# Optimization experiments

Hardware: AMD Instinct MI355X
Metric: run time of the kernel (lower is better)

The kernel has to match this reference:

```python
import jax, jax.numpy as jnp
import numpy as np

BATCH = 4096
P = 64            # num_of_adc_p
L = 1024          # dense_sampling_L
LT = 256          # num_samples_L_tilde


def setup_inputs() -> dict:
    key = jax.random.key(0)
    kx, kw = jax.random.split(key)
    x = jax.random.normal(kx, (BATCH, P * L), dtype=jnp.float32)
    # weight emulates rounded/clamped learned sampling offsets in [1, L-1]
    weight = jax.random.randint(kw, (LT,), 1, L - 1, dtype=jnp.int64)
    return {
        "x": x,
        "weight": weight,
        "num_of_adc_p": P,
        "num_samples_L_tilde": LT,
        "dense_sampling_L": L,
    }


def reference(x, weight, num_of_adc_p, num_samples_L_tilde, dense_sampling_L):
    # out[:, i*LT + j] = x[:, i*L + weight[j]]  -> single fused gather
    # indices: [P, LT] -> flattened column gather
    cols = (jnp.arange(num_of_adc_p, dtype=weight.dtype)[:, None] * dense_sampling_L
            + weight[None, :]).reshape(-1)  # [P*LT]
    return jnp.take(x, cols, axis=1)  # [B, P*LT]
```

## Files before the change

kernel.cpp:

```cpp
#include <hip/hip_runtime.h>
#include <hip/hip_bf16.h>

#define BATCH 4096
#define P     64
#define L     1024
#define LT    256
#define NPAIRS (BATCH * P)

__global__ __launch_bounds__(256, 2)
void HardSamplingLayer_5360119186055_kernel(const float* __restrict__ x,
                                            const int* __restrict__ w,
                                            float* __restrict__ out) {
    __shared__ float tile[L];
    __shared__ int   widx[LT];

    const int t = threadIdx.x;
    widx[t] = w[t];

    int pair = blockIdx.x;
    if (pair >= NPAIRS) return;

    float4 v = ((const float4*)(x + (size_t)pair * L))[t];

    while (pair < NPAIRS) {
        __syncthreads();
        ((float4*)tile)[t] = v;
        __syncthreads();

        const int next = pair + gridDim.x;
        if (next < NPAIRS) {
            v = ((const float4*)(x + (size_t)next * L))[t];
        }

        out[(size_t)pair * LT + t] = tile[widx[t]];

        pair = next;
    }
}

extern "C" void kernel_launch(void* const* d_in, const int* in_sizes, int n_in,
                              void* d_out, int out_size, void* d_ws, size_t ws_size,
                              hipStream_t stream) {
    const float* x = (const float*)d_in[0];
    const int*   w = (const int*)d_in[1];
    float*     out = (float*)d_out;

    dim3 grid(4096), block(256);
    hipLaunchKernelGGL(HardSamplingLayer_5360119186055_kernel,
                       grid, block, 0, stream, x, w, out);
}
```

Measured before the change: 262.7 us.

## Assign one row per wavefront to drop block barriers and vectorize gather stores

Each 64-lane wavefront now handles its own row, with a private LDS tile, instead of the whole block sharing one row. This replaces block-wide __syncthreads with wave barriers. Each lane loads four float4 chunks, reads four weight indices as an int4, and writes a float4 of gathered outputs. The aim is to cut synchronization stalls and issue fewer, wider memory operations. The cost is more LDS per block and reliance on in-wave ordering of LDS accesses.

```diff
diff --git a/kernel.cpp b/kernel.cpp
--- a/kernel.cpp
+++ b/kernel.cpp
@@ -6,33 +6,58 @@
 #define L     1024
 #define LT    256
 #define NPAIRS (BATCH * P)
+#define WPB   4
 
 __global__ __launch_bounds__(256, 2)
 void HardSamplingLayer_5360119186055_kernel(const float* __restrict__ x,
                                             const int* __restrict__ w,
                                             float* __restrict__ out) {
-    __shared__ float tile[L];
-    __shared__ int   widx[LT];
+    __shared__ float tile[WPB][L];
 
-    const int t = threadIdx.x;
-    widx[t] = w[t];
+    const int t  = threadIdx.x & 63;
+    const int wv = threadIdx.x >> 6;
+    float* mytile = tile[wv];
 
-    int pair = blockIdx.x;
+    const int4 wi = ((const int4*)w)[t];
+
+    const int stride = gridDim.x * WPB;
+    int pair = blockIdx.x * WPB + wv;
     if (pair >= NPAIRS) return;
 
-    float4 v = ((const float4*)(x + (size_t)pair * L))[t];
+    {
+        const float4* xp = (const float4*)(x + (size_t)pair * L);
+    }
+    const float4* xp0 = (const float4*)(x + (size_t)pair * L);
+    float4 v0 = xp0[t];
+    float4 v1 = xp0[t + 64];
+    float4 v2 = xp0[t + 128];
+    float4 v3 = xp0[t + 192];
 
     while (pair < NPAIRS) {
-        __syncthreads();
-        ((float4*)tile)[t] = v;
-        __syncthreads();
+        const int next = pair + stride;
 
-        const int next = pair + gridDim.x;
+        ((float4*)mytile)[t]       = v0;
+        ((float4*)mytile)[t + 64]  = v1;
+        ((float4*)mytile)[t + 128] = v2;
+        ((float4*)mytile)[t + 192] = v3;
+        __builtin_amdgcn_wave_barrier();
+
         if (next < NPAIRS) {
-            v = ((const float4*)(x + (size_t)next * L))[t];
+            const float4* xn = (const float4*)(x + (size_t)next * L);
+            v0 = xn[t];
+            v1 = xn[t + 64];
+            v2 = xn[t + 128];
+            v3 = xn[t + 192];
         }
 
-        out[(size_t)pair * LT + t] = tile[widx[t]];
+        float4 o;
+        o.x = mytile[wi.x];
+        o.y = mytile[wi.y];
+        o.z = mytile[wi.z];
+        o.w = mytile[wi.w];
+        __builtin_amdgcn_wave_barrier();
+
+        ((float4*)(out + (size_t)pair * LT))[t] = o;
 
         pair = next;
     }
```

Result: slower. 270.3 us (+2.9%).

## Stage rows per wavefront with async global-to-LDS double buffering

Applied to the files above, without the earlier changes.

Each wavefront now owns a contiguous run of 16 (batch, adc) rows. Rows are copied straight into a per-wave double-buffered LDS tile with global_load_lds, and explicit vmcnt waits replace block-wide __syncthreads. Each lane gathers four samples and writes them with one nontemporal float4 store. The aim is to remove block barriers and register staging and to keep more loads in flight, but it relies on hand-placed waitcnt ordering and on how the builtin handles LDS addresses.

```diff
diff --git a/kernel.cpp b/kernel.cpp
--- a/kernel.cpp
+++ b/kernel.cpp
@@ -6,35 +6,59 @@
 #define L     1024
 #define LT    256
 #define NPAIRS (BATCH * P)
+#define WPB   4
+#define NBLK  4096
+#define PPW   (NPAIRS / (NBLK * WPB))
 
-__global__ __launch_bounds__(256, 2)
+
+typedef const __attribute__((address_space(1))) void* gptr_t;
+typedef __attribute__((address_space(3))) void* lptr_t;
+typedef float nfloat4 __attribute__((ext_vector_type(4)));
+
+__device__ __forceinline__ void stage_tile(const float* gsrc_lane,
+                                           float* lds_base) {
+    __builtin_amdgcn_global_load_lds((gptr_t)(gsrc_lane),        (lptr_t)(lds_base),        16, 0, 0);
+    __builtin_amdgcn_global_load_lds((gptr_t)(gsrc_lane + 256),  (lptr_t)(lds_base + 256),  16, 0, 0);
+    __builtin_amdgcn_global_load_lds((gptr_t)(gsrc_lane + 512),  (lptr_t)(lds_base + 512),  16, 0, 0);
+    __builtin_amdgcn_global_load_lds((gptr_t)(gsrc_lane + 768),  (lptr_t)(lds_base + 768),  16, 0, 0);
+}
+
+__global__ __launch_bounds__(256)
 void HardSamplingLayer_5360119186055_kernel(const float* __restrict__ x,
                                             const int* __restrict__ w,
                                             float* __restrict__ out) {
-    __shared__ float tile[L];
-    __shared__ int   widx[LT];
+    __shared__ float tile[WPB][2][L];
 
-    const int t = threadIdx.x;
-    widx[t] = w[t];
+    const int t  = threadIdx.x & 63;
+    const int wv = threadIdx.x >> 6;
 
-    int pair = blockIdx.x;
-    if (pair >= NPAIRS) return;
+    const int4 wi = ((const int4*)w)[t];
 
-    float4 v = ((const float4*)(x + (size_t)pair * L))[t];
+    const int    wid   = blockIdx.x * WPB + wv;
+    const size_t pair0 = (size_t)wid * PPW;
+    const float* gsrc  = x + pair0 * L + t * 4;
+    float*       gdst  = out + pair0 * LT;
 
-    while (pair < NPAIRS) {
-        __syncthreads();
-        ((float4*)tile)[t] = v;
-        __syncthreads();
+    stage_tile(gsrc, &tile[wv][0][0]);
 
-        const int next = pair + gridDim.x;
-        if (next < NPAIRS) {
-            v = ((const float4*)(x + (size_t)next * L))[t];
+#pragma unroll
+    for (int i = 0; i < PPW; ++i) {
+        const int buf = i & 1;
+        if (i + 1 < PPW) {
+            stage_tile(gsrc + (size_t)(i + 1) * L, &tile[wv][buf ^ 1][0]);
+            asm volatile("s_waitcnt vmcnt(4)" ::: "memory");
+        } else {
+            asm volatile("s_waitcnt vmcnt(0)" ::: "memory");
         }
 
-        out[(size_t)pair * LT + t] = tile[widx[t]];
+        const float* mytile = &tile[wv][buf][0];
+        nfloat4 o;
+        o.x = mytile[wi.x];
+        o.y = mytile[wi.y];
+        o.z = mytile[wi.z];
+        o.w = mytile[wi.w];
 
-        pair = next;
+        __builtin_nontemporal_store(o, (nfloat4*)(gdst + (size_t)i * LT) + t);
     }
 }
 
@@ -45,7 +69,7 @@
     const int*   w = (const int*)d_in[1];
     float*     out = (float*)d_out;
 
-    dim3 grid(4096), block(256);
+    dim3 grid(NBLK), block(256);
     hipLaunchKernelGGL(HardSamplingLayer_5360119186055_kernel,
                        grid, block, 0, stream, x, w, out);
 }
```

Result: no change. 258.1 us (-1.8%).
